# Kernel optimization log

Measured on AMD Instinct MI355X. Metric: run time of the kernel, lower is better.

Reference implementation:

```python
import jax, jax.numpy as jnp
import numpy as np

HIDDEN = 256
HEADS = 4
HEAD_DIM = HIDDEN // HEADS
SCALE = HEAD_DIM ** -0.5
N1, N2 = 6000, 6000


def setup_inputs() -> dict:
    key = jax.random.key(0)
    ks = jax.random.split(key, 12)
    s = 1.0 / np.sqrt(HIDDEN)
    return {
        "kg1_emb": jax.random.normal(ks[0], (N1, HIDDEN), jnp.float32),
        "kg2_emb": jax.random.normal(ks[1], (N2, HIDDEN), jnp.float32),
        "alignment_matrix": jax.random.bernoulli(ks[2], 0.01, (N1, N2)).astype(jnp.float32),
        "Wq": jax.random.normal(ks[3], (HIDDEN, HIDDEN), jnp.float32) * s,
        "bq": jnp.zeros((HIDDEN,), jnp.float32),
        "Wk": jax.random.normal(ks[4], (HIDDEN, HIDDEN), jnp.float32) * s,
        "bk": jnp.zeros((HIDDEN,), jnp.float32),
        "Wv": jax.random.normal(ks[5], (HIDDEN, HIDDEN), jnp.float32) * s,
        "bv": jnp.zeros((HIDDEN,), jnp.float32),
        "Wo": jax.random.normal(ks[6], (HIDDEN, HIDDEN), jnp.float32) * s,
        "bo": jnp.zeros((HIDDEN,), jnp.float32),
    }


def _cross_attend(q_emb, kv_emb, align, Wq, bq, Wk, bk, Wv, bv):
    # q_emb: [Nq, H*D], kv_emb: [Nk, H*D], align: [Nq, Nk]
    Nq, Nk = q_emb.shape[0], kv_emb.shape[0]
    Q = (q_emb @ Wq.T + bq).reshape(Nq, HEADS, HEAD_DIM)
    K = (kv_emb @ Wk.T + bk).reshape(Nk, HEADS, HEAD_DIM)
    V = (kv_emb @ Wv.T + bv).reshape(Nk, HEADS, HEAD_DIM)
    # einsum('nih,mjh->nmij').mean(-1) == Q against head-mean of K (same math)
    Kbar = K.mean(axis=1)  # [Nk, D]
    scores = jnp.einsum('nid,md->nmi', Q, Kbar) * SCALE  # [Nq, Nk, HEADS]
    scores = scores * align[:, :, None]                  # multiplicative mask
    w = jax.nn.softmax(scores, axis=1)                   # over kv entities
    out = jnp.einsum('nmh,mhd->nhd', w, V)               # [Nq, HEADS, D]
    return out.reshape(Nq, HIDDEN)


def reference(kg1_emb, kg2_emb, alignment_matrix, Wq, bq, Wk, bk, Wv, bv, Wo, bo):
    kg1_from_kg2 = _cross_attend(kg1_emb, kg2_emb, alignment_matrix,
                                 Wq, bq, Wk, bk, Wv, bv)
    kg1_enhanced = kg1_emb + (kg1_from_kg2 @ Wo.T + bo)
    kg2_from_kg1 = _cross_attend(kg2_emb, kg1_emb, alignment_matrix.T,
                                 Wq, bq, Wk, bk, Wv, bv)
    kg2_enhanced = kg2_emb + (kg2_from_kg1 @ Wo.T + bo)
    return (kg1_enhanced, kg2_enhanced)
```

## Files before the change

kernel.cpp:

```cpp
#include <hip/hip_runtime.h>
#include <hip/hip_bf16.h>
#include <stdint.h>

typedef __bf16 bf16_t;
typedef __bf16 bf16x8 __attribute__((ext_vector_type(8)));
typedef __bf16 bf16x4 __attribute__((ext_vector_type(4)));
typedef float f32x4 __attribute__((ext_vector_type(4)));

#define NROW 6000
#define HID 256
#define NHEAD 4
#define HD 64
#define ATT_SCALE 0.125f
#define MTOT 12000
#define CAP 128
#define NCHUNK 4500000

__global__ __launch_bounds__(256)
void canon_w_kernel(const float* __restrict__ wq, const float* __restrict__ wk,
                    const float* __restrict__ wv, const float* __restrict__ wo,
                    bf16_t* __restrict__ cW)
{
    int i = blockIdx.x * 256 + threadIdx.x;
    int seg = i >> 16, k = i & 65535;
    const float* s = (seg == 0) ? wq : (seg == 1) ? wk : (seg == 2) ? wv : wo;
    cW[i] = (bf16_t)s[k];
}

__global__ __launch_bounds__(256)
void proj_qkv_kernel(const float* __restrict__ e1, const float* __restrict__ e2,
                     const bf16_t* __restrict__ cW,
                     const float* __restrict__ bq, const float* __restrict__ bk,
                     const float* __restrict__ bv,
                     bf16_t* __restrict__ Q, bf16_t* __restrict__ Kf, bf16_t* __restrict__ V)
{
    int m0   = blockIdx.x * 64;
    int n0   = blockIdx.y * 64;
    int wave = threadIdx.x >> 6;
    int lane = threadIdx.x & 63;
    int r16  = lane & 15;
    int quad = lane >> 4;

    int sel = n0 >> 8;
    int jb  = n0 & 255;
    const bf16_t* W = cW + (size_t)sel * HID * HID;
    const float* bias = (sel == 0) ? bq : (sel == 1) ? bk : bv;

    int arow = m0 + wave * 16 + r16;
    int rr   = arow < MTOT ? arow : MTOT - 1;
    const float* asrc = (rr < NROW) ? (e1 + (size_t)rr * HID)
                                    : (e2 + (size_t)(rr - NROW) * HID);

    f32x4 acc0 = {0,0,0,0}, acc1 = {0,0,0,0}, acc2 = {0,0,0,0}, acc3 = {0,0,0,0};
#pragma unroll
    for (int kk = 0; kk < HID; kk += 32) {
        f32x4 af0 = *(const f32x4*)(asrc + kk + quad * 8);
        f32x4 af1 = *(const f32x4*)(asrc + kk + quad * 8 + 4);
        bf16x8 a;
#pragma unroll
        for (int i = 0; i < 4; ++i) { a[i] = (bf16_t)af0[i]; a[4 + i] = (bf16_t)af1[i]; }
        const bf16_t* b0 = W + (size_t)(jb + r16) * HID + kk + quad * 8;
        bf16x8 f0 = *(const bf16x8*)(b0);
        bf16x8 f1 = *(const bf16x8*)(b0 + 16 * HID);
        bf16x8 f2 = *(const bf16x8*)(b0 + 32 * HID);
        bf16x8 f3 = *(const bf16x8*)(b0 + 48 * HID);
        acc0 = __builtin_amdgcn_mfma_f32_16x16x32_bf16(a, f0, acc0, 0, 0, 0);
        acc1 = __builtin_amdgcn_mfma_f32_16x16x32_bf16(a, f1, acc1, 0, 0, 0);
        acc2 = __builtin_amdgcn_mfma_f32_16x16x32_bf16(a, f2, acc2, 0, 0, 0);
        acc3 = __builtin_amdgcn_mfma_f32_16x16x32_bf16(a, f3, acc3, 0, 0, 0);
    }
    f32x4 accs[4] = {acc0, acc1, acc2, acc3};
    bf16_t* dst = (sel == 0) ? Q : (sel == 1) ? Kf : V;
    int rbase = m0 + wave * 16 + quad * 4;
#pragma unroll
    for (int nt = 0; nt < 4; ++nt) {
        int j = jb + nt * 16 + r16;
        float bb = bias[j];
#pragma unroll
        for (int rg = 0; rg < 4; ++rg) {
            int r = rbase + rg;
            if (r < MTOT)
                dst[(size_t)r * HID + j] = (bf16_t)(accs[nt][rg] + bb);
        }
    }
}

__global__ __launch_bounds__(256)
void kbar_vsum_kernel(const bf16_t* __restrict__ Kf, const bf16_t* __restrict__ V,
                      bf16_t* __restrict__ Kbar, float* __restrict__ Vsum)
{
    int b = blockIdx.x;
    if (b < 3000) {
        int id = b * 256 + threadIdx.x;
        int m = id >> 6, d = id & 63;
        const bf16_t* kr = Kf + (size_t)m * HID + d;
        Kbar[id] = (bf16_t)(0.25f * ((float)kr[0] + (float)kr[64] +
                                     (float)kr[128] + (float)kr[192]));
    } else {
        int idx = b - 3000;
        int g = idx / 24;
        int seg = idx - g * 24;
        int j = threadIdx.x;
        const bf16_t* base = V + ((size_t)(g * NROW + seg * 250)) * HID + j;
        float s = 0.f;
        for (int m = 0; m < 250; ++m) s += (float)base[(size_t)m * HID];
        atomicAdd(Vsum + g * HID + j, s);
    }
}

__global__ __launch_bounds__(256)
void scan_nz_kernel(const float* __restrict__ am,
                    int* __restrict__ rcur,
                    int* __restrict__ csr)
{
    int lane = threadIdx.x & 63;
    int ch   = blockIdx.x * 256 + threadIdx.x;
    bool oob = (ch >= NCHUNK);
    int che  = oob ? (NCHUNK - 1) : ch;

    unsigned int nzmask = 0;
    if (!oob) {
        const unsigned int* aw = (const unsigned int*)am + (size_t)che * 8;
        uint4 u0 = *(const uint4*)(aw);
        uint4 u1 = *(const uint4*)(aw + 4);
        unsigned int any = u0.x | u0.y | u0.z | u0.w | u1.x | u1.y | u1.z | u1.w;
        if (any) {
            unsigned int w[8] = {u0.x, u0.y, u0.z, u0.w, u1.x, u1.y, u1.z, u1.w};
#pragma unroll
            for (int p = 0; p < 8; ++p)
                if (w[p]) nzmask |= 1u << p;
        }
    }
    int n  = che / 750;
    int m0 = (che - n * 750) * 8;
    int c  = __popc(nzmask);

    int p = c;
#pragma unroll
    for (int off = 1; off < 64; off <<= 1) {
        int t = __shfl_up(p, off);
        if (lane >= off) p += t;
    }
    int excl  = p - c;
    int total = __shfl(p, 63);

    int nFirst = __shfl(n, 0);
    int nLast  = __shfl(n, 63);
    unsigned long long mb = __ballot(n == nLast);
    int s0  = __ffsll(mb) - 1;
    int pS0 = __shfl(excl, s0);

    int baseB = 0;
    if (lane == s0) {
        int totalB = total - pS0;
        if (totalB > 0) baseB = atomicAdd(rcur + nLast, totalB);
    }
    baseB = __shfl(baseB, s0);
    int baseA = 0;
    if (s0 > 0) {
        if (lane == 0 && pS0 > 0) baseA = atomicAdd(rcur + nFirst, pS0);
        baseA = __shfl(baseA, 0);
    }

    int myOff = (n == nLast) ? (baseB + excl - pS0) : (baseA + excl);
    if (c) {
        int* dst = csr + (size_t)n * CAP;
        int w = 0;
#pragma unroll
        for (int pb = 0; pb < 8; ++pb) {
            if (nzmask & (1u << pb)) {
                int idx = myOff + (w++);
                if (idx < CAP) dst[idx] = m0 + pb;
            }
        }
    }
}

__global__ __launch_bounds__(256)
void csc_kernel(const int* __restrict__ rcnt, const int* __restrict__ csr,
                int* __restrict__ ccur, int* __restrict__ csc)
{
    int tid = blockIdx.x * 256 + threadIdx.x;
    int n = tid >> 7, j = tid & (CAP - 1);
    if (n >= NROW) return;
    int cnt = rcnt[n]; if (cnt > CAP) cnt = CAP;
    if (j >= cnt) return;
    int m = csr[(size_t)n * CAP + j];
    int slot = atomicAdd(ccur + m, 1);
    if (slot < CAP) csc[(size_t)m * CAP + slot] = n;
}

__global__ __launch_bounds__(256)
void attn_kernel(const bf16_t* __restrict__ Q, const bf16_t* __restrict__ Kbar,
                 const bf16_t* __restrict__ V, const float* __restrict__ Vsum,
                 const int* __restrict__ rcnt, const int* __restrict__ ccnt,
                 const int* __restrict__ csr, const int* __restrict__ csc,
                 bf16_t* __restrict__ att)
{
    __shared__ float qs[HID];
    __shared__ int   ml[CAP];
    __shared__ float sc[CAP * 5];
    __shared__ float w0s[NHEAD];
    __shared__ __align__(16) bf16_t kbs[CAP * HD];

    int dir = blockIdx.y;
    int n   = blockIdx.x;
    int t   = threadIdx.x;
    int wave = t >> 6, lane = t & 63;

    size_t qrow = (size_t)(dir ? NROW + n : n);
    const bf16_t* kb_base = Kbar + (dir ? 0 : (size_t)NROW * HD);
    const bf16_t* v_base  = V    + (dir ? 0 : (size_t)NROW * HID);
    const float*  vs      = Vsum + (dir ? 0 : HID);
    const int*    lst     = (dir ? csc : csr) + (size_t)n * CAP;
    int cnt = (dir ? ccnt : rcnt)[n];
    if (cnt > CAP) cnt = CAP;

    qs[t] = (float)Q[qrow * HID + t];
    for (int j = t; j < cnt; j += 256) ml[j] = lst[j];
    __syncthreads();

    for (int j = wave; j < cnt; j += 4) {
        int m = ml[j];
        bf16_t v = kb_base[(size_t)m * HD + lane];
        kbs[j * HD + ((((lane >> 3) + j) & 7) << 3) + (lane & 7)] = v;
    }
    __syncthreads();

    {
        int head = wave;
        const float* qh = qs + head * HD;
        for (int jb2 = 0; jb2 < cnt; jb2 += 64) {
            int j = jb2 + lane;
            if (j < cnt) {
                float dot = 0.f;
#pragma unroll
                for (int c = 0; c < 8; ++c) {
                    bf16x8 k8 = *(const bf16x8*)(kbs + j * HD + (((c + j) & 7) << 3));
#pragma unroll
                    for (int i = 0; i < 8; ++i)
                        dot += qh[c * 8 + i] * (float)k8[i];
                }
                sc[j * 5 + head] = dot * ATT_SCALE;
            }
        }
    }
    __syncthreads();

    {
        int head = wave;
        float M = 0.0f;
        for (int j = lane; j < cnt; j += 64) M = fmaxf(M, sc[j * 5 + head]);
        for (int off = 32; off; off >>= 1) M = fmaxf(M, __shfl_xor(M, off));
        float e0 = __expf(-M);
        float e[2]; int k = 0;
        float S = 0.f;
        for (int j = lane; j < cnt; j += 64, ++k) { e[k] = __expf(sc[j * 5 + head] - M); S += e[k]; }
        for (int off = 32; off; off >>= 1) S += __shfl_xor(S, off);
        float Z = S + (float)(NROW - cnt) * e0;
        float invZ = 1.0f / Z;
        k = 0;
        for (int j = lane; j < cnt; j += 64, ++k) sc[j * 5 + head] = (e[k] - e0) * invZ;
        if (lane == 0) w0s[head] = e0 * invZ;
    }
    __syncthreads();

    int h3 = lane >> 4;
    int dq = lane & 15;
    int colb = h3 * HD + dq * 4;
    float a0 = 0.f, a1 = 0.f, a2 = 0.f, a3 = 0.f;
    {
        int j = wave;
        for (; j + 4 < cnt; j += 8) {
            int   m0 = ml[j];            int   m1 = ml[j + 4];
            float c0 = sc[j * 5 + h3];   float c1 = sc[(j + 4) * 5 + h3];
            bf16x4 r0 = *(const bf16x4*)(v_base + (size_t)m0 * HID + colb);
            bf16x4 r1 = *(const bf16x4*)(v_base + (size_t)m1 * HID + colb);
            a0 += c0 * (float)r0[0] + c1 * (float)r1[0];
            a1 += c0 * (float)r0[1] + c1 * (float)r1[1];
            a2 += c0 * (float)r0[2] + c1 * (float)r1[2];
            a3 += c0 * (float)r0[3] + c1 * (float)r1[3];
        }
        if (j < cnt) {
            int   m0 = ml[j];
            float c0 = sc[j * 5 + h3];
            bf16x4 r0 = *(const bf16x4*)(v_base + (size_t)m0 * HID + colb);
            a0 += c0 * (float)r0[0];
            a1 += c0 * (float)r0[1];
            a2 += c0 * (float)r0[2];
            a3 += c0 * (float)r0[3];
        }
    }
    __syncthreads();
    float* red = (float*)kbs;
    red[wave * 256 + colb + 0] = a0;
    red[wave * 256 + colb + 1] = a1;
    red[wave * 256 + colb + 2] = a2;
    red[wave * 256 + colb + 3] = a3;
    __syncthreads();
    float tot = red[t] + red[256 + t] + red[512 + t] + red[768 + t]
              + w0s[t >> 6] * vs[t];
    att[qrow * HID + t] = (bf16_t)tot;
}

__global__ __launch_bounds__(256)
void proj_out_kernel(const bf16_t* __restrict__ att, const bf16_t* __restrict__ wo,
                     const float* __restrict__ bo,
                     const float* __restrict__ e1, const float* __restrict__ e2,
                     float* __restrict__ out)
{
    int m0   = blockIdx.x * 64;
    int n0   = blockIdx.y * 64;
    int wave = threadIdx.x >> 6;
    int lane = threadIdx.x & 63;
    int r16  = lane & 15;
    int quad = lane >> 4;

    int arow = m0 + wave * 16 + r16;
    int rr   = arow < MTOT ? arow : MTOT - 1;
    const bf16_t* asrc = att + (size_t)rr * HID;

    f32x4 acc0 = {0,0,0,0}, acc1 = {0,0,0,0}, acc2 = {0,0,0,0}, acc3 = {0,0,0,0};
#pragma unroll
    for (int kk = 0; kk < HID; kk += 32) {
        bf16x8 a = *(const bf16x8*)(asrc + kk + quad * 8);
        const bf16_t* b0 = wo + (size_t)(n0 + r16) * HID + kk + quad * 8;
        bf16x8 f0 = *(const bf16x8*)(b0);
        bf16x8 f1 = *(const bf16x8*)(b0 + 16 * HID);
        bf16x8 f2 = *(const bf16x8*)(b0 + 32 * HID);
        bf16x8 f3 = *(const bf16x8*)(b0 + 48 * HID);
        acc0 = __builtin_amdgcn_mfma_f32_16x16x32_bf16(a, f0, acc0, 0, 0, 0);
        acc1 = __builtin_amdgcn_mfma_f32_16x16x32_bf16(a, f1, acc1, 0, 0, 0);
        acc2 = __builtin_amdgcn_mfma_f32_16x16x32_bf16(a, f2, acc2, 0, 0, 0);
        acc3 = __builtin_amdgcn_mfma_f32_16x16x32_bf16(a, f3, acc3, 0, 0, 0);
    }
    f32x4 accs[4] = {acc0, acc1, acc2, acc3};
    int rbase = m0 + wave * 16 + quad * 4;
#pragma unroll
    for (int nt = 0; nt < 4; ++nt) {
        int j = n0 + nt * 16 + r16;
        float bb = bo[j];
#pragma unroll
        for (int rg = 0; rg < 4; ++rg) {
            int r = rbase + rg;
            if (r < MTOT) {
                const float* emb = (r < NROW) ? (e1 + (size_t)r * HID)
                                              : (e2 + (size_t)(r - NROW) * HID);
                float v = accs[nt][rg] + bb + emb[j];
                out[(size_t)r * HID + j] = v;
            }
        }
    }
}

extern "C" void kernel_launch(void* const* d_in, const int* in_sizes, int n_in,
                              void* d_out, int out_size, void* d_ws, size_t ws_size,
                              hipStream_t stream)
{
    const float* e1 = (const float*)d_in[0];
    const float* e2 = (const float*)d_in[1];
    const float* am = (const float*)d_in[2];
    const float* wq = (const float*)d_in[3];
    const float* bq = (const float*)d_in[4];
    const float* wk = (const float*)d_in[5];
    const float* bk = (const float*)d_in[6];
    const float* wv = (const float*)d_in[7];
    const float* bv = (const float*)d_in[8];
    const float* wo = (const float*)d_in[9];
    const float* bo = (const float*)d_in[10];
    float* out = (float*)d_out;

    size_t off = 0;
    char* base = (char*)d_ws;
    auto alloc = [&](size_t bytes) -> void* {
        void* p = base + off;
        off += (bytes + 255) & ~(size_t)255;
        return p;
    };
    bf16_t* Q    = (bf16_t*)alloc((size_t)MTOT * HID * 2);
    bf16_t* Kf   = (bf16_t*)alloc((size_t)MTOT * HID * 2);
    bf16_t* V    = (bf16_t*)alloc((size_t)MTOT * HID * 2);
    bf16_t* Kbar = (bf16_t*)alloc((size_t)MTOT * HD * 2);
    bf16_t* att  = (bf16_t*)alloc((size_t)MTOT * HID * 2);
    bf16_t* cW   = (bf16_t*)alloc((size_t)4 * HID * HID * 2);
    int*    csr  = (int*)   alloc((size_t)NROW * CAP * 4);
    int*    csc  = (int*)   alloc((size_t)NROW * CAP * 4);
    int*    rcur = (int*)   alloc(NROW * 4);
    int*    ccur = (int*)   alloc(NROW * 4);
    float*  Vsum = (float*) alloc(2 * HID * 4);

    size_t zero_bytes = (size_t)((char*)Vsum - (char*)rcur) + 2 * HID * 4;
    hipMemsetAsync(rcur, 0, zero_bytes, stream);

    canon_w_kernel<<<1024, 256, 0, stream>>>(wq, wk, wv, wo, cW);

    proj_qkv_kernel<<<dim3(188, 12), 256, 0, stream>>>(
        e1, e2, cW, bq, bk, bv, Q, Kf, V);

    kbar_vsum_kernel<<<3048, 256, 0, stream>>>(Kf, V, Kbar, Vsum);

    scan_nz_kernel<<<(NCHUNK + 255) / 256, 256, 0, stream>>>(am, rcur, csr);
    csc_kernel<<<(NROW * CAP) / 256, 256, 0, stream>>>(rcur, csr, ccur, csc);

    attn_kernel<<<dim3(NROW, 2), 256, 0, stream>>>(
        Q, Kbar, V, Vsum, rcur, ccur, csr, csc, att);

    proj_out_kernel<<<dim3(188, 4), 256, 0, stream>>>(att, cW + 3 * HID * HID, bo, e1, e2, out);
}
```

Measured before the change: 421.1 us.

## Compute sparse attention scores with MFMA on gathered Kbar rows

Replaces the shared-memory staging of gathered Kbar rows and the scalar per-lane dot products with bf16 MFMA 16x16x32 instructions. Kbar rows are loaded straight from global memory into A fragments, and Q heads are packed into the B operand, with 12 of its 16 columns zero-padded. This removes a staging pass, one barrier and the large LDS buffer, which may help occupancy. In exchange, most of the MFMA output is wasted, and the barrier before the reduction writes is dropped because red is now a separate buffer.

```diff
diff --git a/kernel.cpp b/kernel.cpp
--- a/kernel.cpp
+++ b/kernel.cpp
@@ -197,11 +197,11 @@
                  const int* __restrict__ csr, const int* __restrict__ csc,
                  bf16_t* __restrict__ att)
 {
-    __shared__ float qs[HID];
+    __shared__ __align__(16) bf16_t qsb[HID];
     __shared__ int   ml[CAP];
     __shared__ float sc[CAP * 5];
     __shared__ float w0s[NHEAD];
-    __shared__ __align__(16) bf16_t kbs[CAP * HD];
+    __shared__ float red[4 * HID];
 
     int dir = blockIdx.y;
     int n   = blockIdx.x;
@@ -216,32 +216,38 @@
     int cnt = (dir ? ccnt : rcnt)[n];
     if (cnt > CAP) cnt = CAP;
 
-    qs[t] = (float)Q[qrow * HID + t];
+    qsb[t] = Q[qrow * HID + t];
     for (int j = t; j < cnt; j += 256) ml[j] = lst[j];
     __syncthreads();
 
-    for (int j = wave; j < cnt; j += 4) {
-        int m = ml[j];
-        bf16_t v = kb_base[(size_t)m * HD + lane];
-        kbs[j * HD + ((((lane >> 3) + j) & 7) << 3) + (lane & 7)] = v;
-    }
-    __syncthreads();
+    int m16  = lane & 15;
+    int quad = lane >> 4;
 
     {
-        int head = wave;
-        const float* qh = qs + head * HD;
-        for (int jb2 = 0; jb2 < cnt; jb2 += 64) {
-            int j = jb2 + lane;
-            if (j < cnt) {
-                float dot = 0.f;
-#pragma unroll
-                for (int c = 0; c < 8; ++c) {
-                    bf16x8 k8 = *(const bf16x8*)(kbs + j * HD + (((c + j) & 7) << 3));
-#pragma unroll
-                    for (int i = 0; i < 8; ++i)
-                        dot += qh[c * 8 + i] * (float)k8[i];
+        bf16x8 b0, b1;
+        if (m16 < NHEAD) {
+            b0 = *(const bf16x8*)(qsb + m16 * HD + 0  + quad * 8);
+            b1 = *(const bf16x8*)(qsb + m16 * HD + 32 + quad * 8);
+        } else {
+            b0 = (bf16x8)(bf16_t)0.f;
+            b1 = (bf16x8)(bf16_t)0.f;
+        }
+        for (int jt = wave; jt * 16 < cnt; jt += 4) {
+            int j  = jt * 16 + m16;
+            int jj = j < cnt ? j : cnt - 1;
+            int row = ml[jj];
+            const bf16_t* ap = kb_base + (size_t)row * HD + quad * 8;
+            bf16x8 a0 = *(const bf16x8*)(ap);
+            bf16x8 a1 = *(const bf16x8*)(ap + 32);
+            f32x4 acc = {0, 0, 0, 0};
+            acc = __builtin_amdgcn_mfma_f32_16x16x32_bf16(a0, b0, acc, 0, 0, 0);
+            acc = __builtin_amdgcn_mfma_f32_16x16x32_bf16(a1, b1, acc, 0, 0, 0);
+            if (m16 < NHEAD) {
+#pragma unroll
+                for (int rg = 0; rg < 4; ++rg) {
+                    int jw = jt * 16 + quad * 4 + rg;
+                    if (jw < cnt) sc[jw * 5 + m16] = acc[rg] * ATT_SCALE;
                 }
-                sc[j * 5 + head] = dot * ATT_SCALE;
             }
         }
     }
@@ -291,8 +297,6 @@
             a3 += c0 * (float)r0[3];
         }
     }
-    __syncthreads();
-    float* red = (float*)kbs;
     red[wave * 256 + colb + 0] = a0;
     red[wave * 256 + colb + 1] = a1;
     red[wave * 256 + colb + 2] = a2;
```

After: 387.0 us. 8.1% less time.
